# Optimization experiments

Hardware: AMD Instinct MI355X
Metric: run time of the kernel (lower is better)

## Reference

```python
import jax, jax.numpy as jnp
import numpy as np

Nh = 128
B = 4096


def _conv3d(x, w):
    # x: [B, C, D, H, W], w: [O, I, 3, 3, 3], same padding, no bias
    return jax.lax.conv_general_dilated(
        x, w, window_strides=(1, 1, 1), padding=[(1, 1)] * 3,
        dimension_numbers=("NCDHW", "OIDHW", "NCDHW"))


def setup_inputs() -> dict:
    key = jax.random.key(0)
    ks = jax.random.split(key, 12)
    x = jax.random.normal(ks[0], (B, 1024), dtype=jnp.float32)
    hidden_states = jax.random.normal(ks[1], (B, Nh, 4, 4, 4), dtype=jnp.float32)
    cw = 0.05  # small init for conv kernels
    Wz = jax.random.normal(ks[2], (Nh, Nh, 3, 3, 3), dtype=jnp.float32) * cw
    Wr = jax.random.normal(ks[3], (Nh, Nh, 3, 3, 3), dtype=jnp.float32) * cw
    Wm = jax.random.normal(ks[4], (Nh, Nh, 3, 3, 3), dtype=jnp.float32) * cw
    # biases init like np.random.rand -> uniform [0,1)
    bz = jax.random.uniform(ks[5], (1, Nh, 4, 4, 4), dtype=jnp.float32)
    br = jax.random.uniform(ks[6], (1, Nh, 4, 4, 4), dtype=jnp.float32)
    bm = jax.random.uniform(ks[7], (1, Nh, 4, 4, 4), dtype=jnp.float32)
    lw = 0.03
    Lz = jax.random.normal(ks[8], (Nh * 64, 1024), dtype=jnp.float32) * lw
    Lr = jax.random.normal(ks[9], (Nh * 64, 1024), dtype=jnp.float32) * lw
    Lm = jax.random.normal(ks[10], (Nh * 64, 1024), dtype=jnp.float32) * lw
    return dict(x=x, hidden_states=hidden_states, Wz=Wz, Wr=Wr, Wm=Wm,
                bz=bz, br=br, bm=bm, Lz=Lz, Lr=Lr, Lm=Lm)


def reference(x, hidden_states, Wz, Wr, Wm, bz, br, bm, Lz, Lr, Lm):
    # linear projections (torch Linear: x @ W.T), reshaped to voxel grid
    lz = (x @ Lz.T).reshape(B, Nh, 4, 4, 4)
    lr = (x @ Lr.T).reshape(B, Nh, 4, 4, 4)
    lm = (x @ Lm.T).reshape(B, Nh, 4, 4, 4)
    z = jax.nn.sigmoid(_conv3d(hidden_states, Wz) + lz + bz)
    r = jax.nn.sigmoid(_conv3d(hidden_states, Wr) + lr + br)
    mem = jnp.tanh(_conv3d(r * hidden_states, Wm) + lm + bm)
    return (1.0 - z) * hidden_states + z * mem
```

## Files before the change

### kernel.cpp

```cpp
#include <hip/hip_runtime.h>
#include <cstdint>

typedef __attribute__((ext_vector_type(8))) short bf16x8;
typedef __attribute__((ext_vector_type(4))) float f32x4;
typedef unsigned short u16;
typedef unsigned int u32;

static const size_t OFF_WT = 0;
static const size_t OFF_XB = 2654464;
static const size_t OFF_LB = 11043072;
static const size_t OFF_HT = 61374720;
static const size_t OFF_RH = 128483584;

__device__ __forceinline__ u16 f2bf(float x) {
  union { float f; u32 u; } v; v.f = x;
  u32 r = (v.u + 0x7FFFu + ((v.u >> 16) & 1u)) >> 16;
  return (u16)r;
}
__device__ __forceinline__ float bf2f(u16 x) {
  union { u32 u; float f; } v; v.u = ((u32)x) << 16; return v.f;
}

__device__ __forceinline__ void gload16(const void* g, void* l) {
  __builtin_amdgcn_global_load_lds(
      (const __attribute__((address_space(1))) uint32_t*)g,
      (__attribute__((address_space(3))) uint32_t*)l, 16, 0, 0);
}

__global__ __launch_bounds__(256) void k_cvt(
    const float* __restrict__ x,
    const float* __restrict__ Wz, const float* __restrict__ Wr, const float* __restrict__ Wm,
    const float* __restrict__ Lz, const float* __restrict__ Lr, const float* __restrict__ Lm,
    uint8_t* __restrict__ ws) {
  u16* wt = (u16*)(ws + OFF_WT);
  u16* xb = (u16*)(ws + OFF_XB);
  u16* lb = (u16*)(ws + OFF_LB);
  const long NWT = 3L * 27 * 128 * 128;
  const long NX  = 4096L * 1024;
  const long NL  = 3L * 8192 * 1024;
  const long total = NWT + NX + NL;
  for (long i = (long)blockIdx.x * blockDim.x + threadIdx.x; i < total;
       i += (long)gridDim.x * blockDim.x) {
    if (i < NWT) {
      long g = i / (27L * 16384);
      long r = i % (27L * 16384);
      long t = r / 16384;
      long oc = (r / 128) % 128;
      long ic = r % 128;
      const float* W = (g == 0) ? Wz : ((g == 1) ? Wr : Wm);
      wt[i] = f2bf(W[(oc * 128 + ic) * 27 + t]);
    } else if (i < NWT + NX) {
      long j = i - NWT;
      xb[j] = f2bf(x[j]);
    } else {
      long j = i - NWT - NX;
      long g = j / (8192L * 1024);
      long r = j % (8192L * 1024);
      const float* L = (g == 0) ? Lz : ((g == 1) ? Lr : Lm);
      lb[j] = f2bf(L[r]);
    }
  }
}

__global__ __launch_bounds__(256) void k_ht(const float* __restrict__ h, uint8_t* __restrict__ ws) {
  __shared__ float tile[128 * 65];
  int b = blockIdx.x;
  const float* hb = h + (size_t)b * 8192;
  u16* ht = (u16*)(ws + OFF_HT) + (size_t)b * 8192;
  for (int i = threadIdx.x; i < 8192; i += 256) {
    int ic = i >> 6, vo = i & 63;
    tile[ic * 65 + vo] = hb[i];
  }
  __syncthreads();
  for (int i = threadIdx.x; i < 8192; i += 256) {
    int vo = i >> 7, ic = i & 127;
    ht[i] = f2bf(tile[ic * 65 + vo]);
  }
}

template <int MODE>
__global__ __launch_bounds__(512, 2) void k_conv_gemm(
    uint8_t* __restrict__ ws,
    const float* __restrict__ bz, const float* __restrict__ br, const float* __restrict__ bm,
    u32* __restrict__ dout) {
  int bx = blockIdx.x;
  int g, vo, mb;
  if (MODE == 0) { mb = bx & 15; g = (bx >> 4) & 1; vo = bx >> 5; }
  else           { mb = bx & 15; g = 2;             vo = bx >> 4; }

  const uint8_t* wt_b = ws + OFF_WT + (size_t)g * 27 * 32768;
  const uint8_t* xb_b = ws + OFF_XB;
  const uint8_t* lb_b = ws + OFF_LB + (size_t)g * 8192 * 2048;
  const uint8_t* as_b = ws + ((MODE == 0) ? OFF_HT : OFF_RH);

  __shared__ __align__(1024) uint8_t lds[3 * 49152];

  const int tid = threadIdx.x;
  const int w = tid >> 6;
  const int l = tid & 63;
  const int lrow = l >> 3;
  const int co = (((l & 7) ^ lrow) << 4);
  const int wm = (w >> 1) * 64;
  const int wn = (w & 1) * 64;
  const int lr16 = l & 15;
  const int lk = l >> 4;

  f32x4 acc[4][4];
#pragma unroll
  for (int m = 0; m < 4; ++m)
#pragma unroll
    for (int n = 0; n < 4; ++n) acc[m][n] = (f32x4){0.f, 0.f, 0.f, 0.f};

  const uint8_t* aA_x = xb_b + ((size_t)(mb * 256 + w * 32 + lrow)) * 2048 + co;
  const uint8_t* aA_t = as_b + ((size_t)(mb * 256 + w * 32 + lrow)) * 16384 + co;
  const uint8_t* aB_x = lb_b + ((size_t)(w * 16 + lrow)) * 131072 + (size_t)vo * 2048 + co;
  const uint8_t* aB_t = wt_b + ((size_t)(w * 16 + lrow)) * 256 + co;

  const int d = vo >> 4, e = (vo >> 2) & 3, f = vo & 3;
  auto validT = [&](int t) {
    int p3 = t / 9 - 1, q3 = (t / 3) % 3 - 1, s3 = t % 3 - 1;
    int dd = d + p3, ee = e + q3, ff = f + s3;
    return dd >= 0 && dd <= 3 && ee >= 0 && ee <= 3 && ff >= 0 && ff <= 3;
  };
  const int nd = 3 - (d == 0) - (d == 3);
  const int ne = 3 - (e == 0) - (e == 3);
  const int nf = 3 - (f == 0) - (f == 3);
  const int NP = 16 + 2 * nd * ne * nf;

  int s_kt = 0;
  int s_t = 0, s_ih = 0;
  while (!validT(s_t)) ++s_t;

  auto stage_next = [&](int buf) {
    uint8_t* Ad = lds + buf * 49152 + w * 4096;
    uint8_t* Bd = lds + buf * 49152 + 32768 + w * 2048;
    if (s_kt < 16) {
      int kt = s_kt;
#pragma unroll
      for (int i = 0; i < 4; ++i)
        gload16(aA_x + (size_t)kt * 128 + i * 16384, Ad + i * 1024);
#pragma unroll
      for (int j = 0; j < 2; ++j)
        gload16(aB_x + (size_t)kt * 128 + (size_t)j * 1048576, Bd + j * 1024);
      ++s_kt;
    } else {
      int t = s_t, ih = s_ih;
      int dd = d + t / 9 - 1, ee = e + (t / 3) % 3 - 1, ff = f + t % 3 - 1;
      int vi = dd * 16 + ee * 4 + ff;
#pragma unroll
      for (int i = 0; i < 4; ++i)
        gload16(aA_t + (size_t)vi * 256 + ih * 128 + i * 131072, Ad + i * 1024);
#pragma unroll
      for (int j = 0; j < 2; ++j)
        gload16(aB_t + (size_t)t * 32768 + ih * 128 + j * 2048, Bd + j * 1024);
      s_ih ^= 1;
      if (!s_ih) { do { ++s_t; } while (s_t < 27 && !validT(s_t)); }
    }
  };

  auto compute = [&](int buf) {
    const u16* At = (const u16*)(lds + buf * 49152);
    const u16* Bt = (const u16*)(lds + buf * 49152 + 32768);
#pragma unroll
    for (int ks = 0; ks < 2; ++ks) {
      bf16x8 af[4], bfr[4];
#pragma unroll
      for (int m = 0; m < 4; ++m) {
        int row = wm + m * 16 + lr16;
        int c = ks * 4 + lk;
        af[m] = *(const bf16x8*)&At[row * 64 + ((c ^ (row & 7)) * 8)];
      }
#pragma unroll
      for (int n = 0; n < 4; ++n) {
        int row = wn + n * 16 + lr16;
        int c = ks * 4 + lk;
        bfr[n] = *(const bf16x8*)&Bt[row * 64 + ((c ^ (row & 7)) * 8)];
      }
#pragma unroll
      for (int m = 0; m < 4; ++m)
#pragma unroll
        for (int n = 0; n < 4; ++n)
          acc[m][n] = __builtin_amdgcn_mfma_f32_16x16x32_bf16(af[m], bfr[n], acc[m][n], 0, 0, 0);
    }
  };

  stage_next(0);
  stage_next(1);
  int cb = 0, sb = 2;
  for (int p = 0; p < NP; ++p) {
    if (p + 1 < NP) asm volatile("s_waitcnt vmcnt(6)" ::: "memory");
    else            asm volatile("s_waitcnt vmcnt(0)" ::: "memory");
    __builtin_amdgcn_s_barrier();
    if (p + 2 < NP) stage_next(sb);
    compute(cb);
    cb = (cb == 2) ? 0 : cb + 1;
    sb = (sb == 2) ? 0 : sb + 1;
  }

  const float* bias = (MODE == 0) ? ((g == 0) ? bz : br) : bm;
  const u16* htp = (const u16*)(ws + OFF_HT);
  u16* rhp = (u16*)(ws + OFF_RH);
#pragma unroll
  for (int n = 0; n < 4; ++n) {
    int oc = wn + n * 16 + lr16;
    float bv = bias[oc * 64 + vo];
#pragma unroll
    for (int m = 0; m < 4; ++m) {
#pragma unroll
      for (int j = 0; j < 4; ++j) {
        int brow = mb * 256 + wm + m * 16 + lk * 4 + j;
        size_t pidx = (size_t)brow * 8192 + (size_t)vo * 128 + oc;
        float pre = acc[m][n][j] + bv;
        pre = fminf(fmaxf(pre, -30.f), 30.f);
        if (MODE == 0) {
          float sg = 1.f / (1.f + __expf(-pre));
          if (g == 0) {
            dout[pidx] = (u32)f2bf(sg);
          } else {
            float hv = bf2f(htp[pidx]);
            rhp[pidx] = f2bf(sg * hv);
          }
        } else {
          float e2 = __expf(-2.f * pre);
          float th = (1.f - e2) / (1.f + e2);
          u32 old = dout[pidx];
          dout[pidx] = (old & 0xFFFFu) | (((u32)f2bf(th)) << 16);
        }
      }
    }
  }
}

__global__ __launch_bounds__(256) void k_combine(const float* __restrict__ h, u32* __restrict__ dout) {
  __shared__ u32 tile[64 * 129];
  int b = blockIdx.x;
  const u32* db = dout + (size_t)b * 8192;
  for (int i = threadIdx.x; i < 8192; i += 256) {
    int vo = i >> 7, oc = i & 127;
    tile[vo * 129 + oc] = db[i];
  }
  __syncthreads();
  float* ob = (float*)dout + (size_t)b * 8192;
  const float* hb = h + (size_t)b * 8192;
  for (int o = threadIdx.x; o < 8192; o += 256) {
    int oc = o >> 6, vo = o & 63;
    u32 pk = tile[vo * 129 + oc];
    float z = bf2f((u16)(pk & 0xFFFFu));
    float mem = bf2f((u16)(pk >> 16));
    ob[o] = (1.f - z) * hb[o] + z * mem;
  }
}

extern "C" void kernel_launch(void* const* d_in, const int* in_sizes, int n_in,
                              void* d_out, int out_size, void* d_ws, size_t ws_size,
                              hipStream_t stream) {
  const float* x  = (const float*)d_in[0];
  const float* h  = (const float*)d_in[1];
  const float* Wz = (const float*)d_in[2];
  const float* Wr = (const float*)d_in[3];
  const float* Wm = (const float*)d_in[4];
  const float* bz = (const float*)d_in[5];
  const float* br = (const float*)d_in[6];
  const float* bm = (const float*)d_in[7];
  const float* Lz = (const float*)d_in[8];
  const float* Lr = (const float*)d_in[9];
  const float* Lm = (const float*)d_in[10];
  uint8_t* ws = (uint8_t*)d_ws;
  u32* dout = (u32*)d_out;

  k_cvt<<<2048, 256, 0, stream>>>(x, Wz, Wr, Wm, Lz, Lr, Lm, ws);
  k_ht<<<4096, 256, 0, stream>>>(h, ws);
  k_conv_gemm<0><<<2048, 512, 0, stream>>>(ws, bz, br, bm, dout);
  k_conv_gemm<1><<<1024, 512, 0, stream>>>(ws, bz, br, bm, dout);
  k_combine<<<4096, 256, 0, stream>>>(h, dout);
}
```

Measured before the change: 945.6 us.

## Split K-loop into two half-phases interleaving staging, LDS reads and MFMA with setprio

```diff
diff --git a/kernel.cpp b/kernel.cpp
--- a/kernel.cpp
+++ b/kernel.cpp
@@ -131,69 +131,94 @@
   int s_t = 0, s_ih = 0;
   while (!validT(s_t)) ++s_t;
 
-  auto stage_next = [&](int buf) {
-    uint8_t* Ad = lds + buf * 49152 + w * 4096;
-    uint8_t* Bd = lds + buf * 49152 + 32768 + w * 2048;
+  auto stage_half = [&](int buf, int half) {
+    uint8_t* Ad = lds + buf * 49152 + w * 4096 + half * 2048;
+    uint8_t* Bd = lds + buf * 49152 + 32768 + w * 2048 + half * 1024;
     if (s_kt < 16) {
       int kt = s_kt;
 #pragma unroll
-      for (int i = 0; i < 4; ++i)
-        gload16(aA_x + (size_t)kt * 128 + i * 16384, Ad + i * 1024);
-#pragma unroll
-      for (int j = 0; j < 2; ++j)
-        gload16(aB_x + (size_t)kt * 128 + (size_t)j * 1048576, Bd + j * 1024);
-      ++s_kt;
+      for (int i = 0; i < 2; ++i)
+        gload16(aA_x + (size_t)kt * 128 + (size_t)(half * 2 + i) * 16384, Ad + i * 1024);
+      gload16(aB_x + (size_t)kt * 128 + (size_t)half * 1048576, Bd);
+      if (half) ++s_kt;
     } else {
       int t = s_t, ih = s_ih;
       int dd = d + t / 9 - 1, ee = e + (t / 3) % 3 - 1, ff = f + t % 3 - 1;
       int vi = dd * 16 + ee * 4 + ff;
 #pragma unroll
-      for (int i = 0; i < 4; ++i)
-        gload16(aA_t + (size_t)vi * 256 + ih * 128 + i * 131072, Ad + i * 1024);
-#pragma unroll
-      for (int j = 0; j < 2; ++j)
-        gload16(aB_t + (size_t)t * 32768 + ih * 128 + j * 2048, Bd + j * 1024);
-      s_ih ^= 1;
-      if (!s_ih) { do { ++s_t; } while (s_t < 27 && !validT(s_t)); }
+      for (int i = 0; i < 2; ++i)
+        gload16(aA_t + (size_t)vi * 256 + ih * 128 + (size_t)(half * 2 + i) * 131072, Ad + i * 1024);
+      gload16(aB_t + (size_t)t * 32768 + ih * 128 + (size_t)half * 2048, Bd);
+      if (half) {
+        s_ih ^= 1;
+        if (!s_ih) { do { ++s_t; } while (s_t < 27 && !validT(s_t)); }
+      }
     }
   };
 
-  auto compute = [&](int buf) {
-    const u16* At = (const u16*)(lds + buf * 49152);
-    const u16* Bt = (const u16*)(lds + buf * 49152 + 32768);
-#pragma unroll
-    for (int ks = 0; ks < 2; ++ks) {
-      bf16x8 af[4], bfr[4];
-#pragma unroll
-      for (int m = 0; m < 4; ++m) {
+  stage_half(0, 0); stage_half(0, 1);
+  stage_half(1, 0); stage_half(1, 1);
+  asm volatile("s_waitcnt vmcnt(6)" ::: "memory");
+  __builtin_amdgcn_s_barrier();
+
+  int cur = 0, sb = 2;
+  for (int p = 0; p < NP; ++p) {
+    const u16* At = (const u16*)(lds + cur * 49152);
+    const u16* Bt = (const u16*)(lds + cur * 49152 + 32768);
+    bf16x8 afA[2][2], afB[2][2], bfr[4][2];
+
+#pragma unroll
+    for (int m = 0; m < 2; ++m)
+#pragma unroll
+      for (int ks = 0; ks < 2; ++ks) {
         int row = wm + m * 16 + lr16;
         int c = ks * 4 + lk;
-        af[m] = *(const bf16x8*)&At[row * 64 + ((c ^ (row & 7)) * 8)];
-      }
-#pragma unroll
-      for (int n = 0; n < 4; ++n) {
+        afA[m][ks] = *(const bf16x8*)&At[row * 64 + ((c ^ (row & 7)) * 8)];
+      }
+#pragma unroll
+    for (int n = 0; n < 4; ++n)
+#pragma unroll
+      for (int ks = 0; ks < 2; ++ks) {
         int row = wn + n * 16 + lr16;
         int c = ks * 4 + lk;
-        bfr[n] = *(const bf16x8*)&Bt[row * 64 + ((c ^ (row & 7)) * 8)];
-      }
-#pragma unroll
-      for (int m = 0; m < 4; ++m)
-#pragma unroll
-        for (int n = 0; n < 4; ++n)
-          acc[m][n] = __builtin_amdgcn_mfma_f32_16x16x32_bf16(af[m], bfr[n], acc[m][n], 0, 0, 0);
-    }
-  };
-
-  stage_next(0);
-  stage_next(1);
-  int cb = 0, sb = 2;
-  for (int p = 0; p < NP; ++p) {
-    if (p + 1 < NP) asm volatile("s_waitcnt vmcnt(6)" ::: "memory");
-    else            asm volatile("s_waitcnt vmcnt(0)" ::: "memory");
+        bfr[n][ks] = *(const bf16x8*)&Bt[row * 64 + ((c ^ (row & 7)) * 8)];
+      }
+    if (p + 2 < NP) stage_half(sb, 0);
     __builtin_amdgcn_s_barrier();
-    if (p + 2 < NP) stage_next(sb);
-    compute(cb);
-    cb = (cb == 2) ? 0 : cb + 1;
+    __builtin_amdgcn_s_setprio(1);
+#pragma unroll
+    for (int m = 0; m < 2; ++m)
+#pragma unroll
+      for (int n = 0; n < 4; ++n)
+#pragma unroll
+        for (int ks = 0; ks < 2; ++ks)
+          acc[m][n] = __builtin_amdgcn_mfma_f32_16x16x32_bf16(afA[m][ks], bfr[n][ks], acc[m][n], 0, 0, 0);
+    __builtin_amdgcn_s_setprio(0);
+    __builtin_amdgcn_s_barrier();
+
+#pragma unroll
+    for (int m = 0; m < 2; ++m)
+#pragma unroll
+      for (int ks = 0; ks < 2; ++ks) {
+        int row = wm + (m + 2) * 16 + lr16;
+        int c = ks * 4 + lk;
+        afB[m][ks] = *(const bf16x8*)&At[row * 64 + ((c ^ (row & 7)) * 8)];
+      }
+    if (p + 2 < NP) stage_half(sb, 1);
+    __builtin_amdgcn_s_barrier();
+    __builtin_amdgcn_s_setprio(1);
+#pragma unroll
+    for (int m = 0; m < 2; ++m)
+#pragma unroll
+      for (int n = 0; n < 4; ++n)
+#pragma unroll
+        for (int ks = 0; ks < 2; ++ks)
+          acc[m + 2][n] = __builtin_amdgcn_mfma_f32_16x16x32_bf16(afB[m][ks], bfr[n][ks], acc[m + 2][n], 0, 0, 0);
+    __builtin_amdgcn_s_setprio(0);
+    if (p + 2 < NP)      asm volatile("s_waitcnt vmcnt(6)" ::: "memory");
+    else if (p + 1 < NP) asm volatile("s_waitcnt vmcnt(0)" ::: "memory");
+    __builtin_amdgcn_s_barrier();
+    cur = (cur == 2) ? 0 : cur + 1;
     sb = (sb == 2) ? 0 : sb + 1;
   }
 
```

New measurement: 1.028 ms. +8.8%, slower.
